# Optimization experiments

Measured on AMD Instinct MI355X. Metric: run time of the kernel, lower is better.

Reference implementation:

```python
import math
import jax, jax.numpy as jnp
import numpy as np

B, S, D = 4, 2048, 1024
L = 2                      # codec_decoder_transformer_lengths entry
H, HD = 8, 128             # n_heads == n_kv_heads (no GQA repeat)
FF = 4096
WINDOW = 16                # sliding window (causal: keys in [i-16, i])
NORM_EPS = 0.01
QK_EPS = 1e-6
SCALE_INIT = 0.1           # layer_id < 18 -> 0.1


def _alibi_slopes(n):
    # n is a power of 2 here (8)
    r = 2.0 ** (-8.0 / n)
    return jnp.array([r ** (i + 1) for i in range(n)], dtype=jnp.float32)


def rms_norm(x, w, eps):
    return x * jax.lax.rsqrt(jnp.mean(x * x, axis=-1, keepdims=True) + eps) * w


def _attn_bias(dtype):
    pos = jnp.arange(S)
    rel = pos[None, :] - pos[:, None]          # [S,S], rel = j - i
    slopes = _alibi_slopes(H).astype(dtype)
    bias = slopes[:, None, None] * rel[None].astype(dtype)   # [H,S,S]
    mask = (rel > 0) | (rel < -WINDOW)         # causal + sliding window
    return jnp.where(mask[None], -jnp.inf, bias)


def setup_inputs() -> dict:
    key = jax.random.key(0)
    ks = jax.random.split(key, 9)
    sd = 0.02
    w = lambda k, shape: jax.random.normal(k, shape, jnp.float32) * sd
    return {
        "x": jax.random.normal(ks[0], (B, S, D), jnp.float32),
        "wq": w(ks[1], (L, D, H * HD)),
        "wk": w(ks[2], (L, D, H * HD)),
        "wv": w(ks[3], (L, D, H * HD)),
        "wo": w(ks[4], (L, H * HD, D)),
        "q_norm_w": jnp.ones((L, H * HD), jnp.float32),
        "k_norm_w": jnp.ones((L, H * HD), jnp.float32),
        "w1": w(ks[5], (L, D, FF)),
        "w2": w(ks[6], (L, FF, D)),
        "w3": w(ks[7], (L, D, FF)),
        "attn_norm_w": jnp.ones((L, D), jnp.float32),
        "ffn_norm_w": jnp.ones((L, D), jnp.float32),
        "attn_scale": jnp.full((L, D), SCALE_INIT, jnp.float32),
        "ffn_scale": jnp.full((L, D), SCALE_INIT, jnp.float32),
    }


def reference(x, wq, wk, wv, wo, q_norm_w, k_norm_w, w1, w2, w3,
              attn_norm_w, ffn_norm_w, attn_scale, ffn_scale):
    bias = _attn_bias(x.dtype)                 # [H,S,S]
    inv_sqrt_d = 1.0 / math.sqrt(HD)

    def block(h, p):
        (lwq, lwk, lwv, lwo, qnw, knw, lw1, lw2, lw3, anw, fnw, asc, fsc) = p
        xn = rms_norm(h, anw, NORM_EPS)
        # qk_norm applied on the flat (H*HD) projection before the head split
        q = rms_norm(xn @ lwq, qnw, QK_EPS).reshape(B, S, H, HD).transpose(0, 2, 1, 3)
        k = rms_norm(xn @ lwk, knw, QK_EPS).reshape(B, S, H, HD).transpose(0, 2, 1, 3)
        v = (xn @ lwv).reshape(B, S, H, HD).transpose(0, 2, 1, 3)
        scores = jnp.einsum('bhqd,bhkd->bhqk', q, k) * inv_sqrt_d + bias[None]
        attn = jax.nn.softmax(scores, axis=-1)
        y = jnp.einsum('bhqk,bhkd->bhqd', attn, v)
        y = y.transpose(0, 2, 1, 3).reshape(B, S, H * HD)
        h = h + asc * (y @ lwo)
        xn = rms_norm(h, fnw, NORM_EPS)
        ff = (jax.nn.silu(xn @ lw1) * (xn @ lw3)) @ lw2
        return h + fsc * ff, None

    out, _ = jax.lax.scan(
        block, x,
        (wq, wk, wv, wo, q_norm_w, k_norm_w, w1, w2, w3,
         attn_norm_w, ffn_norm_w, attn_scale, ffn_scale))
    return out
```

## Files before the change

kernel.cpp:

```cpp
#include <hip/hip_runtime.h>

#define B_ 4
#define S_ 2048
#define D_ 1024
#define H_ 8
#define HD_ 128
#define FF_ 4096
#define R_ (B_*S_)

typedef __attribute__((ext_vector_type(8))) short short8;
typedef __attribute__((ext_vector_type(4))) float f32x4;

__device__ __forceinline__ unsigned short f2bf(float f) {
  unsigned int u = __float_as_uint(f);
  return (unsigned short)((u + 0x7fffu + ((u >> 16) & 1u)) >> 16);
}
__device__ __forceinline__ float bf2f(unsigned short s) {
  return __uint_as_float(((unsigned int)s) << 16);
}

typedef const __attribute__((address_space(1))) unsigned int* gas_p;
typedef __attribute__((address_space(3))) unsigned int* las_p;
__device__ __forceinline__ void gload16(const void* g, void* l) {
  __builtin_amdgcn_global_load_lds((gas_p)g, (las_p)l, 16, 0, 0);
}

__global__ __launch_bounds__(256) void f2bf_t(const float* __restrict__ src,
    unsigned short* __restrict__ dst, int Rows, int Cols) {
  __shared__ float tile[32][33];
  const int tx = threadIdx.x & 31, ty = threadIdx.x >> 5;
  const int r0 = blockIdx.y * 32, c0 = blockIdx.x * 32;
  #pragma unroll
  for (int j = 0; j < 32; j += 8)
    tile[ty + j][tx] = src[(size_t)(r0 + ty + j) * Cols + c0 + tx];
  __syncthreads();
  #pragma unroll
  for (int j = 0; j < 32; j += 8)
    dst[(size_t)(c0 + ty + j) * Rows + r0 + tx] = f2bf(tile[tx][ty + j]);
}

__global__ __launch_bounds__(256) void rmsnorm_f2b(const float* __restrict__ in,
    const float* __restrict__ w, unsigned short* __restrict__ out, float eps) {
  const int row = blockIdx.x, t = threadIdx.x;
  const float4 xv = *(const float4*)&in[(size_t)row * D_ + t * 4];
  float p = xv.x*xv.x + xv.y*xv.y + xv.z*xv.z + xv.w*xv.w;
  #pragma unroll
  for (int off = 32; off >= 1; off >>= 1) p += __shfl_xor(p, off);
  __shared__ float red[4];
  if ((t & 63) == 0) red[t >> 6] = p;
  __syncthreads();
  float scl = rsqrtf((red[0] + red[1] + red[2] + red[3]) * (1.0f / D_) + eps);
  const float4 wv = *(const float4*)&w[t * 4];
  ((ushort4*)out)[(size_t)row * 256 + t] = make_ushort4(
      f2bf(xv.x*scl*wv.x), f2bf(xv.y*scl*wv.y), f2bf(xv.z*scl*wv.z), f2bf(xv.w*scl*wv.w));
}

__global__ __launch_bounds__(256) void qknorm_k(unsigned short* __restrict__ qkv,
    const float* __restrict__ qw, const float* __restrict__ kw) {
  const int row = blockIdx.x, t = threadIdx.x;
  unsigned short* qp = qkv + (size_t)row * 3072;
  unsigned short* kp = qp + 1024;
  const ushort4 qv = ((const ushort4*)qp)[t];
  const ushort4 kv = ((const ushort4*)kp)[t];
  float q0 = bf2f(qv.x), q1 = bf2f(qv.y), q2 = bf2f(qv.z), q3 = bf2f(qv.w);
  float k0 = bf2f(kv.x), k1 = bf2f(kv.y), k2 = bf2f(kv.z), k3 = bf2f(kv.w);
  float pq = q0*q0 + q1*q1 + q2*q2 + q3*q3;
  float pk = k0*k0 + k1*k1 + k2*k2 + k3*k3;
  #pragma unroll
  for (int off = 32; off >= 1; off >>= 1) { pq += __shfl_xor(pq, off); pk += __shfl_xor(pk, off); }
  __shared__ float redq[4], redk[4];
  if ((t & 63) == 0) { redq[t >> 6] = pq; redk[t >> 6] = pk; }
  __syncthreads();
  float sq = rsqrtf((redq[0]+redq[1]+redq[2]+redq[3]) * (1.0f / D_) + 1e-6f);
  float sk = rsqrtf((redk[0]+redk[1]+redk[2]+redk[3]) * (1.0f / D_) + 1e-6f);
  const float4 qwv = *(const float4*)&qw[t * 4];
  const float4 kwv = *(const float4*)&kw[t * 4];
  ((ushort4*)qp)[t] = make_ushort4(f2bf(q0*sq*qwv.x), f2bf(q1*sq*qwv.y),
                                   f2bf(q2*sq*qwv.z), f2bf(q3*sq*qwv.w));
  ((ushort4*)kp)[t] = make_ushort4(f2bf(k0*sk*kwv.x), f2bf(k1*sk*kwv.y),
                                   f2bf(k2*sk*kwv.z), f2bf(k3*sk*kwv.w));
}

__global__ __launch_bounds__(256) void attn_k(const unsigned short* __restrict__ qkv,
    unsigned short* __restrict__ y) {
  const int lane = threadIdx.x & 63;
  const int wid = (blockIdx.x * 256 + threadIdx.x) >> 6;
  const int i  = wid & (S_ - 1);
  const int bh = wid >> 11;
  const int hh = bh & (H_ - 1);
  const int b  = bh >> 3;
  const float slope = exp2f(-(float)(hh + 1));
  const float inv = 0.088388347648318447f;
  const size_t rowq = ((size_t)(b * S_ + i)) * 3072 + hh * HD_ + lane * 2;
  const ushort2 qv = *(const ushort2*)&qkv[rowq];
  const float qx = bf2f(qv.x), qy = bf2f(qv.y);
  float sc[17];
  #pragma unroll
  for (int jj = 0; jj < 17; ++jj) {
    int j = i - 16 + jj;
    int jc = j < 0 ? 0 : j;
    size_t koff = ((size_t)(b * S_ + jc)) * 3072 + 1024 + hh * HD_ + lane * 2;
    ushort2 kv = *(const ushort2*)&qkv[koff];
    float p = qx * bf2f(kv.x) + qy * bf2f(kv.y);
    p += __shfl_xor(p, 32); p += __shfl_xor(p, 16); p += __shfl_xor(p, 8);
    p += __shfl_xor(p, 4);  p += __shfl_xor(p, 2);  p += __shfl_xor(p, 1);
    sc[jj] = (j >= 0) ? (p * inv + slope * (float)(jj - 16)) : -1e30f;
  }
  float m = sc[0];
  #pragma unroll
  for (int jj = 1; jj < 17; ++jj) m = fmaxf(m, sc[jj]);
  float wsum = 0.f, ax = 0.f, ay = 0.f;
  #pragma unroll
  for (int jj = 0; jj < 17; ++jj) {
    int j = i - 16 + jj;
    int jc = j < 0 ? 0 : j;
    float wgt = expf(sc[jj] - m);
    size_t voff = ((size_t)(b * S_ + jc)) * 3072 + 2048 + hh * HD_ + lane * 2;
    ushort2 vv = *(const ushort2*)&qkv[voff];
    wsum += wgt; ax += wgt * bf2f(vv.x); ay += wgt * bf2f(vv.y);
  }
  float rs = 1.f / wsum;
  size_t yoff = ((size_t)(b * S_ + i)) * 1024 + hh * HD_ + lane * 2;
  *(ushort2*)&y[yoff] = make_ushort2(f2bf(ax * rs), f2bf(ay * rs));
}

template<int EPI>
__global__ __launch_bounds__(512, 2) void gemm256(
    const unsigned short* __restrict__ A, const unsigned short* __restrict__ Bt,
    void* __restrict__ Cout, const float* __restrict__ sc, int M, int N, int K) {
  __shared__ __align__(16) unsigned short lds[2][2][16384];
  const int t = threadIdx.x;
  const int lane = t & 63, w = t >> 6;
  const int wm = w >> 2, wn = w & 3;
  const int lr = lane & 15, lk = lane >> 4;
  const int xm = lr & 7;

  const int nbx = N >> 8;
  const int nwg = gridDim.x;
  const int bid = blockIdx.x;
  const int swz = (bid & 7) * (nwg >> 3) + (bid >> 3);
  const int br = (swz / nbx) << 8;
  const int bc = (swz % nbx) << 8;

  const unsigned short* Abase = A + (size_t)br * K;
  const unsigned short* Bbase = Bt + (size_t)bc * K;

  auto stageA = [&](int buf, int u, int k0) {
    #pragma unroll
    for (int j = 0; j < 2; ++j) {
      int gr = (t + (j << 9)) >> 3, slot = t & 7;
      int row = ((gr & 63) | ((gr >> 6) << 7)) + (u << 6);
      gload16(Abase + (size_t)row * K + k0 + ((slot ^ (row & 7)) << 3),
              &lds[buf][0][row * 64 + slot * 8]);
    }
  };
  auto stageB = [&](int buf, int u, int k0) {
    #pragma unroll
    for (int j = 0; j < 2; ++j) {
      int gr = (t + (j << 9)) >> 3, slot = t & 7;
      int row = ((gr & 31) | ((gr >> 5) << 6)) + (u << 5);
      gload16(Bbase + (size_t)row * K + k0 + ((slot ^ (row & 7)) << 3),
              &lds[buf][1][row * 64 + slot * 8]);
    }
  };

  f32x4 acc[8][4];
  #pragma unroll
  for (int mi = 0; mi < 8; ++mi)
    #pragma unroll
    for (int ni = 0; ni < 4; ++ni) { f32x4 z = {0.f,0.f,0.f,0.f}; acc[mi][ni] = z; }

  const int NT = K >> 6;
  stageA(0, 0, 0); stageB(0, 0, 0); stageA(0, 1, 0); stageB(0, 1, 0);
  asm volatile("s_waitcnt vmcnt(0)" ::: "memory");
  __builtin_amdgcn_s_barrier();

  for (int kt = 0; kt < NT; ++kt) {
    const int cur = kt & 1, nxt = cur ^ 1;
    const int kp = (kt + 1 < NT) ? ((kt + 1) << 6) : 0;
    const unsigned short* Al = lds[cur][0];
    const unsigned short* Bl = lds[cur][1];
    short8 af[4][2], bfA[2][2], bfB[2][2];

    #pragma unroll
    for (int mf = 0; mf < 4; ++mf)
      #pragma unroll
      for (int ks = 0; ks < 2; ++ks)
        af[mf][ks] = *(const short8*)&Al[(wm*128 + mf*16 + lr)*64 + (((ks*4+lk)^xm)<<3)];
    #pragma unroll
    for (int nf = 0; nf < 2; ++nf)
      #pragma unroll
      for (int ks = 0; ks < 2; ++ks)
        bfA[nf][ks] = *(const short8*)&Bl[(wn*64 + nf*16 + lr)*64 + (((ks*4+lk)^xm)<<3)];
    stageA(nxt, 0, kp);
    asm volatile("s_waitcnt vmcnt(2)" ::: "memory");
    __builtin_amdgcn_s_barrier();
    asm volatile("s_waitcnt lgkmcnt(0)" ::: "memory");
    __builtin_amdgcn_sched_barrier(0);
    __builtin_amdgcn_s_setprio(1);
    #pragma unroll
    for (int mf = 0; mf < 4; ++mf)
      #pragma unroll
      for (int nf = 0; nf < 2; ++nf)
        #pragma unroll
        for (int ks = 0; ks < 2; ++ks)
          acc[mf][nf] = __builtin_amdgcn_mfma_f32_16x16x32_bf16(af[mf][ks], bfA[nf][ks], acc[mf][nf], 0, 0, 0);
    __builtin_amdgcn_s_setprio(0);
    __builtin_amdgcn_s_barrier();

    #pragma unroll
    for (int nf = 0; nf < 2; ++nf)
      #pragma unroll
      for (int ks = 0; ks < 2; ++ks)
        bfB[nf][ks] = *(const short8*)&Bl[(wn*64 + (nf+2)*16 + lr)*64 + (((ks*4+lk)^xm)<<3)];
    stageB(nxt, 0, kp);
    __builtin_amdgcn_s_barrier();
    asm volatile("s_waitcnt lgkmcnt(0)" ::: "memory");
    __builtin_amdgcn_sched_barrier(0);
    __builtin_amdgcn_s_setprio(1);
    #pragma unroll
    for (int mf = 0; mf < 4; ++mf)
      #pragma unroll
      for (int nf = 0; nf < 2; ++nf)
        #pragma unroll
        for (int ks = 0; ks < 2; ++ks)
          acc[mf][nf+2] = __builtin_amdgcn_mfma_f32_16x16x32_bf16(af[mf][ks], bfB[nf][ks], acc[mf][nf+2], 0, 0, 0);
    __builtin_amdgcn_s_setprio(0);
    __builtin_amdgcn_s_barrier();

    #pragma unroll
    for (int mf = 0; mf < 4; ++mf)
      #pragma unroll
      for (int ks = 0; ks < 2; ++ks)
        af[mf][ks] = *(const short8*)&Al[(wm*128 + (mf+4)*16 + lr)*64 + (((ks*4+lk)^xm)<<3)];
    stageA(nxt, 1, kp);
    __builtin_amdgcn_s_barrier();
    asm volatile("s_waitcnt lgkmcnt(0)" ::: "memory");
    __builtin_amdgcn_sched_barrier(0);
    __builtin_amdgcn_s_setprio(1);
    #pragma unroll
    for (int mf = 0; mf < 4; ++mf)
      #pragma unroll
      for (int nf = 0; nf < 2; ++nf)
        #pragma unroll
        for (int ks = 0; ks < 2; ++ks)
          acc[mf+4][nf+2] = __builtin_amdgcn_mfma_f32_16x16x32_bf16(af[mf][ks], bfB[nf][ks], acc[mf+4][nf+2], 0, 0, 0);
    __builtin_amdgcn_s_setprio(0);
    __builtin_amdgcn_s_barrier();

    #pragma unroll
    for (int nf = 0; nf < 2; ++nf)
      #pragma unroll
      for (int ks = 0; ks < 2; ++ks)
        bfA[nf][ks] = *(const short8*)&Bl[(wn*64 + nf*16 + lr)*64 + (((ks*4+lk)^xm)<<3)];
    stageB(nxt, 1, kp);
    asm volatile("s_waitcnt vmcnt(4)" ::: "memory");
    __builtin_amdgcn_s_barrier();
    asm volatile("s_waitcnt lgkmcnt(0)" ::: "memory");
    __builtin_amdgcn_sched_barrier(0);
    __builtin_amdgcn_s_setprio(1);
    #pragma unroll
    for (int mf = 0; mf < 4; ++mf)
      #pragma unroll
      for (int nf = 0; nf < 2; ++nf)
        #pragma unroll
        for (int ks = 0; ks < 2; ++ks)
          acc[mf+4][nf] = __builtin_amdgcn_mfma_f32_16x16x32_bf16(af[mf][ks], bfA[nf][ks], acc[mf+4][nf], 0, 0, 0);
    __builtin_amdgcn_s_setprio(0);
    __builtin_amdgcn_s_barrier();
  }

  if (EPI == 0) {
    unsigned short* C = (unsigned short*)Cout;
    #pragma unroll
    for (int mf = 0; mf < 8; ++mf)
      #pragma unroll
      for (int nf = 0; nf < 4; ++nf) {
        int row = br + wm*128 + mf*16 + lk*4;
        int col = bc + wn*64 + nf*16 + lr;
        #pragma unroll
        for (int r = 0; r < 4; ++r)
          C[(size_t)(row + r) * N + col] = f2bf(acc[mf][nf][r]);
      }
  } else {
    float* hp = (float*)Cout;
    #pragma unroll
    for (int nf = 0; nf < 4; ++nf) {
      int col = bc + wn*64 + nf*16 + lr;
      float sv = sc[col];
      #pragma unroll
      for (int mf = 0; mf < 8; ++mf) {
        int row = br + wm*128 + mf*16 + lk*4;
        #pragma unroll
        for (int r = 0; r < 4; ++r)
          hp[(size_t)(row + r) * N + col] += sv * acc[mf][nf][r];
      }
    }
  }
}

__device__ __forceinline__ void stage_tile(const unsigned short* __restrict__ src,
    unsigned short* lds, int rowbase, int K, int k0, int t) {
  #pragma unroll
  for (int it = 0; it < 4; ++it) {
    int g = it * 256 + t;
    int row = g >> 3, slot = g & 7;
    int sc8 = (slot ^ (row & 7)) << 3;
    gload16(&src[(size_t)(rowbase + row) * K + k0 + sc8], &lds[g * 8]);
  }
}

__global__ __launch_bounds__(256, 2) void gemm_w13(
    const unsigned short* __restrict__ A, const unsigned short* __restrict__ B1t,
    const unsigned short* __restrict__ B3t, unsigned short* __restrict__ G,
    int M, int N, int K) {
  __shared__ __align__(16) unsigned short As[128 * 64];
  __shared__ __align__(16) unsigned short B1s[128 * 64];
  __shared__ __align__(16) unsigned short B3s[128 * 64];
  const int t = threadIdx.x;
  const int lane = t & 63, w = t >> 6;
  const int wr = w >> 1, wc = w & 1;
  const int br = blockIdx.y * 128, bc = blockIdx.x * 128;
  const int lr = lane & 15, lk = lane >> 4;
  const int xm = lr & 7;
  f32x4 acc1[4][4], acc3[4][4];
  #pragma unroll
  for (int mi = 0; mi < 4; ++mi)
    #pragma unroll
    for (int ni = 0; ni < 4; ++ni) {
      f32x4 z = {0.f,0.f,0.f,0.f}; acc1[mi][ni] = z; acc3[mi][ni] = z;
    }
  for (int k0 = 0; k0 < K; k0 += 64) {
    stage_tile(A,   As,  br, K, k0, t);
    stage_tile(B1t, B1s, bc, K, k0, t);
    stage_tile(B3t, B3s, bc, K, k0, t);
    __syncthreads();
    #pragma unroll
    for (int kk = 0; kk < 2; ++kk) {
      short8 af[4], b1r[4], b3r[4];
      #pragma unroll
      for (int mi = 0; mi < 4; ++mi)
        af[mi] = *(const short8*)&As[(wr*64 + mi*16 + lr) * 64 + (((kk*4 + lk) ^ xm) << 3)];
      #pragma unroll
      for (int ni = 0; ni < 4; ++ni) {
        b1r[ni] = *(const short8*)&B1s[(wc*64 + ni*16 + lr) * 64 + (((kk*4 + lk) ^ xm) << 3)];
        b3r[ni] = *(const short8*)&B3s[(wc*64 + ni*16 + lr) * 64 + (((kk*4 + lk) ^ xm) << 3)];
      }
      #pragma unroll
      for (int mi = 0; mi < 4; ++mi)
        #pragma unroll
        for (int ni = 0; ni < 4; ++ni) {
          acc1[mi][ni] = __builtin_amdgcn_mfma_f32_16x16x32_bf16(af[mi], b1r[ni], acc1[mi][ni], 0, 0, 0);
          acc3[mi][ni] = __builtin_amdgcn_mfma_f32_16x16x32_bf16(af[mi], b3r[ni], acc3[mi][ni], 0, 0, 0);
        }
    }
    __syncthreads();
  }
  #pragma unroll
  for (int mi = 0; mi < 4; ++mi)
    #pragma unroll
    for (int ni = 0; ni < 4; ++ni) {
      int row = br + wr * 64 + mi * 16 + lk * 4;
      int col = bc + wc * 64 + ni * 16 + lr;
      #pragma unroll
      for (int r = 0; r < 4; ++r) {
        float a1 = acc1[mi][ni][r], a3 = acc3[mi][ni][r];
        G[(size_t)(row + r) * N + col] = f2bf(a1 / (1.f + expf(-a1)) * a3);
      }
    }
}

extern "C" void kernel_launch(void* const* d_in, const int* in_sizes, int n_in,
                              void* d_out, int out_size, void* d_ws, size_t ws_size,
                              hipStream_t stream) {
  const float* x    = (const float*)d_in[0];
  const float* wq   = (const float*)d_in[1];
  const float* wk   = (const float*)d_in[2];
  const float* wv   = (const float*)d_in[3];
  const float* wo   = (const float*)d_in[4];
  const float* qnw  = (const float*)d_in[5];
  const float* knw  = (const float*)d_in[6];
  const float* w1   = (const float*)d_in[7];
  const float* w2   = (const float*)d_in[8];
  const float* w3   = (const float*)d_in[9];
  const float* anw  = (const float*)d_in[10];
  const float* fnw  = (const float*)d_in[11];
  const float* asc  = (const float*)d_in[12];
  const float* fsc  = (const float*)d_in[13];

  const size_t MB = 1024 * 1024;
  if (ws_size < 144 * MB) return;

  float* h = (float*)d_out;
  char* ws = (char*)d_ws;
  unsigned short* qkvt = (unsigned short*)ws;
  unsigned short* wot  = qkvt + 2u * 3145728u;
  unsigned short* w1t  = wot  + 2u * 1048576u;
  unsigned short* w3t  = w1t  + 2u * 4194304u;
  unsigned short* w2t  = w3t  + 2u * 4194304u;
  unsigned short* xn   = (unsigned short*)(ws + 64 * MB);
  unsigned short* qkv  = (unsigned short*)(ws + 80 * MB);
  unsigned short* gate = qkv;

  hipMemcpyAsync(h, x, (size_t)R_ * D_ * sizeof(float), hipMemcpyDeviceToDevice, stream);

  for (int l = 0; l < 2; ++l) {
    unsigned short* qkvt_l = qkvt + (size_t)l * 3145728u;
    f2bf_t<<<dim3(32, 32),  256, 0, stream>>>(wq + (size_t)l*1048576, qkvt_l,            1024, 1024);
    f2bf_t<<<dim3(32, 32),  256, 0, stream>>>(wk + (size_t)l*1048576, qkvt_l + 1048576,  1024, 1024);
    f2bf_t<<<dim3(32, 32),  256, 0, stream>>>(wv + (size_t)l*1048576, qkvt_l + 2097152,  1024, 1024);
    f2bf_t<<<dim3(32, 32),  256, 0, stream>>>(wo + (size_t)l*1048576, wot + (size_t)l*1048576, 1024, 1024);
    f2bf_t<<<dim3(128, 32), 256, 0, stream>>>(w1 + (size_t)l*4194304, w1t + (size_t)l*4194304, 1024, 4096);
    f2bf_t<<<dim3(128, 32), 256, 0, stream>>>(w3 + (size_t)l*4194304, w3t + (size_t)l*4194304, 1024, 4096);
    f2bf_t<<<dim3(32, 128), 256, 0, stream>>>(w2 + (size_t)l*4194304, w2t + (size_t)l*4194304, 4096, 1024);
  }

  for (int l = 0; l < 2; ++l) {
    rmsnorm_f2b<<<R_, 256, 0, stream>>>(h, anw + l * D_, xn, 0.01f);
    gemm256<0><<<384, 512, 0, stream>>>(xn, qkvt + (size_t)l*3145728u, qkv, nullptr,
                                        R_, 3072, 1024);
    qknorm_k<<<R_, 256, 0, stream>>>(qkv, qnw + l * 1024, knw + l * 1024);
    attn_k<<<R_ * H_ / 4, 256, 0, stream>>>(qkv, xn);
    gemm256<1><<<128, 512, 0, stream>>>(xn, wot + (size_t)l*1048576u, h, asc + l * D_,
                                        R_, 1024, 1024);
    rmsnorm_f2b<<<R_, 256, 0, stream>>>(h, fnw + l * D_, xn, 0.01f);
    gemm_w13<<<dim3(32, 64), 256, 0, stream>>>(xn, w1t + (size_t)l*4194304u,
                                               w3t + (size_t)l*4194304u, gate, R_, 4096, 1024);
    gemm256<1><<<128, 512, 0, stream>>>(gate, w2t + (size_t)l*4194304u, h, fsc + l * D_,
                                        R_, 1024, 4096);
  }
}
```

Baseline: 1.016 ms.

## Merge weight conversions, shrink GEMM tiles to 256x128, rewrite W13 GEMM, drop memcpy

Replaces the fourteen per-matrix weight transpose/convert launches with a single kernel that covers both layers. The main GEMM tile changes from 256x256 to 256x128, which doubles the number of workgroups for the narrow N=1024 projections and gives a simpler double-buffered pipeline. The gated FFN GEMM gets a new 256x128 double-buffered version using direct global-to-LDS loads in place of the single-buffered 128x128 kernel. The initial x->h device copy is removed: layer 0 reads x directly and a new epilogue writes h = x + scale*acc. The smaller tiles trade more A-operand reloading for better occupancy and load balance.

```diff
diff --git a/kernel.cpp b/kernel.cpp
--- a/kernel.cpp
+++ b/kernel.cpp
@@ -25,11 +25,37 @@
   __builtin_amdgcn_global_load_lds((gas_p)g, (las_p)l, 16, 0, 0);
 }
 
-__global__ __launch_bounds__(256) void f2bf_t(const float* __restrict__ src,
-    unsigned short* __restrict__ dst, int Rows, int Cols) {
+__global__ __launch_bounds__(256) void f2bf_t_all(
+    const float* __restrict__ wq, const float* __restrict__ wk,
+    const float* __restrict__ wv, const float* __restrict__ wo,
+    const float* __restrict__ w1, const float* __restrict__ w3,
+    const float* __restrict__ w2,
+    unsigned short* __restrict__ qkvt, unsigned short* __restrict__ wot,
+    unsigned short* __restrict__ w1t, unsigned short* __restrict__ w3t,
+    unsigned short* __restrict__ w2t) {
+  const int id = blockIdx.x;
+  const int l = id >> 14, r = id & 16383;
+  const float* src; unsigned short* dst; int Rows, Cols, t2;
+  if (r < 4096) {
+    Rows = 1024; Cols = 1024; t2 = r & 1023;
+    const int wsel = r >> 10;
+    if (wsel == 0)      { src = wq + (size_t)l*1048576u; dst = qkvt + (size_t)l*3145728u; }
+    else if (wsel == 1) { src = wk + (size_t)l*1048576u; dst = qkvt + (size_t)l*3145728u + 1048576u; }
+    else if (wsel == 2) { src = wv + (size_t)l*1048576u; dst = qkvt + (size_t)l*3145728u + 2097152u; }
+    else                { src = wo + (size_t)l*1048576u; dst = wot + (size_t)l*1048576u; }
+  } else if (r < 12288) {
+    Rows = 1024; Cols = 4096; t2 = (r - 4096) & 4095;
+    if (r < 8192) { src = w1 + (size_t)l*4194304u; dst = w1t + (size_t)l*4194304u; }
+    else          { src = w3 + (size_t)l*4194304u; dst = w3t + (size_t)l*4194304u; }
+  } else {
+    Rows = 4096; Cols = 1024; t2 = r - 12288;
+    src = w2 + (size_t)l*4194304u; dst = w2t + (size_t)l*4194304u;
+  }
+  const int lgc = (Cols == 4096) ? 7 : 5;
+  const int bx = t2 & ((1 << lgc) - 1), by = t2 >> lgc;
+  const int r0 = by * 32, c0 = bx * 32;
   __shared__ float tile[32][33];
   const int tx = threadIdx.x & 31, ty = threadIdx.x >> 5;
-  const int r0 = blockIdx.y * 32, c0 = blockIdx.x * 32;
   #pragma unroll
   for (int j = 0; j < 32; j += 8)
     tile[ty + j][tx] = src[(size_t)(r0 + ty + j) * Cols + c0 + tx];
@@ -127,20 +153,22 @@
 template<int EPI>
 __global__ __launch_bounds__(512, 2) void gemm256(
     const unsigned short* __restrict__ A, const unsigned short* __restrict__ Bt,
-    void* __restrict__ Cout, const float* __restrict__ sc, int M, int N, int K) {
-  __shared__ __align__(16) unsigned short lds[2][2][16384];
+    void* __restrict__ Cout, const float* __restrict__ sc,
+    const float* __restrict__ x2, int M, int N, int K) {
+  __shared__ __align__(16) unsigned short ldsA[2][256 * 64];
+  __shared__ __align__(16) unsigned short ldsB[2][128 * 64];
   const int t = threadIdx.x;
   const int lane = t & 63, w = t >> 6;
   const int wm = w >> 2, wn = w & 3;
   const int lr = lane & 15, lk = lane >> 4;
   const int xm = lr & 7;
 
-  const int nbx = N >> 8;
+  const int nbx = N >> 7;
   const int nwg = gridDim.x;
   const int bid = blockIdx.x;
   const int swz = (bid & 7) * (nwg >> 3) + (bid >> 3);
   const int br = (swz / nbx) << 8;
-  const int bc = (swz % nbx) << 8;
+  const int bc = (swz % nbx) << 7;
 
   const unsigned short* Abase = A + (size_t)br * K;
   const unsigned short* Bbase = Bt + (size_t)bc * K;
@@ -148,52 +176,52 @@
   auto stageA = [&](int buf, int u, int k0) {
     #pragma unroll
     for (int j = 0; j < 2; ++j) {
-      int gr = (t + (j << 9)) >> 3, slot = t & 7;
+      int idx = t + (j << 9);
+      int gr = idx >> 3, slot = idx & 7;
       int row = ((gr & 63) | ((gr >> 6) << 7)) + (u << 6);
       gload16(Abase + (size_t)row * K + k0 + ((slot ^ (row & 7)) << 3),
-              &lds[buf][0][row * 64 + slot * 8]);
+              &ldsA[buf][row * 64 + slot * 8]);
     }
   };
-  auto stageB = [&](int buf, int u, int k0) {
+  auto stageB = [&](int buf, int k0) {
     #pragma unroll
     for (int j = 0; j < 2; ++j) {
-      int gr = (t + (j << 9)) >> 3, slot = t & 7;
-      int row = ((gr & 31) | ((gr >> 5) << 6)) + (u << 5);
+      int idx = t + (j << 9);
+      int row = idx >> 3, slot = idx & 7;
       gload16(Bbase + (size_t)row * K + k0 + ((slot ^ (row & 7)) << 3),
-              &lds[buf][1][row * 64 + slot * 8]);
+              &ldsB[buf][row * 64 + slot * 8]);
     }
   };
 
-  f32x4 acc[8][4];
+  f32x4 acc[8][2];
   #pragma unroll
   for (int mi = 0; mi < 8; ++mi)
     #pragma unroll
-    for (int ni = 0; ni < 4; ++ni) { f32x4 z = {0.f,0.f,0.f,0.f}; acc[mi][ni] = z; }
+    for (int ni = 0; ni < 2; ++ni) { f32x4 z = {0.f,0.f,0.f,0.f}; acc[mi][ni] = z; }
 
   const int NT = K >> 6;
-  stageA(0, 0, 0); stageB(0, 0, 0); stageA(0, 1, 0); stageB(0, 1, 0);
+  stageA(0, 0, 0); stageB(0, 0); stageA(0, 1, 0);
   asm volatile("s_waitcnt vmcnt(0)" ::: "memory");
   __builtin_amdgcn_s_barrier();
 
   for (int kt = 0; kt < NT; ++kt) {
     const int cur = kt & 1, nxt = cur ^ 1;
     const int kp = (kt + 1 < NT) ? ((kt + 1) << 6) : 0;
-    const unsigned short* Al = lds[cur][0];
-    const unsigned short* Bl = lds[cur][1];
-    short8 af[4][2], bfA[2][2], bfB[2][2];
-
-    #pragma unroll
-    for (int mf = 0; mf < 4; ++mf)
-      #pragma unroll
-      for (int ks = 0; ks < 2; ++ks)
-        af[mf][ks] = *(const short8*)&Al[(wm*128 + mf*16 + lr)*64 + (((ks*4+lk)^xm)<<3)];
-    #pragma unroll
-    for (int nf = 0; nf < 2; ++nf)
-      #pragma unroll
-      for (int ks = 0; ks < 2; ++ks)
-        bfA[nf][ks] = *(const short8*)&Bl[(wn*64 + nf*16 + lr)*64 + (((ks*4+lk)^xm)<<3)];
-    stageA(nxt, 0, kp);
-    asm volatile("s_waitcnt vmcnt(2)" ::: "memory");
+    const unsigned short* Al = ldsA[cur];
+    const unsigned short* Bl = ldsB[cur];
+    short8 af[2][4], bfr[2][2];
+
+    #pragma unroll
+    for (int ks = 0; ks < 2; ++ks) {
+      #pragma unroll
+      for (int mf = 0; mf < 4; ++mf)
+        af[ks][mf] = *(const short8*)&Al[(wm*128 + mf*16 + lr)*64 + (((ks*4+lk)^xm)<<3)];
+      #pragma unroll
+      for (int nf = 0; nf < 2; ++nf)
+        bfr[ks][nf] = *(const short8*)&Bl[(wn*32 + nf*16 + lr)*64 + (((ks*4+lk)^xm)<<3)];
+    }
+    stageA(nxt, 0, kp); stageB(nxt, kp); stageA(nxt, 1, kp);
+    asm volatile("s_waitcnt vmcnt(6)" ::: "memory");
     __builtin_amdgcn_s_barrier();
     asm volatile("s_waitcnt lgkmcnt(0)" ::: "memory");
     __builtin_amdgcn_sched_barrier(0);
@@ -204,16 +232,16 @@
       for (int nf = 0; nf < 2; ++nf)
         #pragma unroll
         for (int ks = 0; ks < 2; ++ks)
-          acc[mf][nf] = __builtin_amdgcn_mfma_f32_16x16x32_bf16(af[mf][ks], bfA[nf][ks], acc[mf][nf], 0, 0, 0);
+          acc[mf][nf] = __builtin_amdgcn_mfma_f32_16x16x32_bf16(af[ks][mf], bfr[ks][nf], acc[mf][nf], 0, 0, 0);
     __builtin_amdgcn_s_setprio(0);
     __builtin_amdgcn_s_barrier();
 
     #pragma unroll
-    for (int nf = 0; nf < 2; ++nf)
-      #pragma unroll
-      for (int ks = 0; ks < 2; ++ks)
-        bfB[nf][ks] = *(const short8*)&Bl[(wn*64 + (nf+2)*16 + lr)*64 + (((ks*4+lk)^xm)<<3)];
-    stageB(nxt, 0, kp);
+    for (int ks = 0; ks < 2; ++ks)
+      #pragma unroll
+      for (int mf = 0; mf < 4; ++mf)
+        af[ks][mf] = *(const short8*)&Al[(wm*128 + (mf+4)*16 + lr)*64 + (((ks*4+lk)^xm)<<3)];
+    asm volatile("s_waitcnt vmcnt(2)" ::: "memory");
     __builtin_amdgcn_s_barrier();
     asm volatile("s_waitcnt lgkmcnt(0)" ::: "memory");
     __builtin_amdgcn_sched_barrier(0);
@@ -224,16 +252,133 @@
       for (int nf = 0; nf < 2; ++nf)
         #pragma unroll
         for (int ks = 0; ks < 2; ++ks)
-          acc[mf][nf+2] = __builtin_amdgcn_mfma_f32_16x16x32_bf16(af[mf][ks], bfB[nf][ks], acc[mf][nf+2], 0, 0, 0);
+          acc[mf+4][nf] = __builtin_amdgcn_mfma_f32_16x16x32_bf16(af[ks][mf], bfr[ks][nf], acc[mf+4][nf], 0, 0, 0);
     __builtin_amdgcn_s_setprio(0);
     __builtin_amdgcn_s_barrier();
-
-    #pragma unroll
-    for (int mf = 0; mf < 4; ++mf)
-      #pragma unroll
-      for (int ks = 0; ks < 2; ++ks)
-        af[mf][ks] = *(const short8*)&Al[(wm*128 + (mf+4)*16 + lr)*64 + (((ks*4+lk)^xm)<<3)];
+  }
+
+  if (EPI == 0) {
+    unsigned short* C = (unsigned short*)Cout;
+    #pragma unroll
+    for (int mf = 0; mf < 8; ++mf)
+      #pragma unroll
+      for (int nf = 0; nf < 2; ++nf) {
+        int row = br + wm*128 + mf*16 + lk*4;
+        int col = bc + wn*32 + nf*16 + lr;
+        #pragma unroll
+        for (int r = 0; r < 4; ++r)
+          C[(size_t)(row + r) * N + col] = f2bf(acc[mf][nf][r]);
+      }
+  } else if (EPI == 1) {
+    float* hp = (float*)Cout;
+    #pragma unroll
+    for (int nf = 0; nf < 2; ++nf) {
+      int col = bc + wn*32 + nf*16 + lr;
+      float sv = sc[col];
+      #pragma unroll
+      for (int mf = 0; mf < 8; ++mf) {
+        int row = br + wm*128 + mf*16 + lk*4;
+        #pragma unroll
+        for (int r = 0; r < 4; ++r)
+          hp[(size_t)(row + r) * N + col] += sv * acc[mf][nf][r];
+      }
+    }
+  } else {
+    float* hp = (float*)Cout;
+    #pragma unroll
+    for (int nf = 0; nf < 2; ++nf) {
+      int col = bc + wn*32 + nf*16 + lr;
+      float sv = sc[col];
+      #pragma unroll
+      for (int mf = 0; mf < 8; ++mf) {
+        int row = br + wm*128 + mf*16 + lk*4;
+        #pragma unroll
+        for (int r = 0; r < 4; ++r)
+          hp[(size_t)(row + r) * N + col] = x2[(size_t)(row + r) * N + col] + sv * acc[mf][nf][r];
+      }
+    }
+  }
+}
+
+__global__ __launch_bounds__(512, 2) void gemm_w13_256(
+    const unsigned short* __restrict__ A, const unsigned short* __restrict__ B1t,
+    const unsigned short* __restrict__ B3t, unsigned short* __restrict__ G,
+    int M, int N, int K) {
+  __shared__ __align__(16) unsigned short ldsA[2][256 * 64];
+  __shared__ __align__(16) unsigned short ldsB1[2][128 * 64];
+  __shared__ __align__(16) unsigned short ldsB3[2][128 * 64];
+  const int t = threadIdx.x;
+  const int lane = t & 63, w = t >> 6;
+  const int wm = w >> 2, wn = w & 3;
+  const int lr = lane & 15, lk = lane >> 4;
+  const int xm = lr & 7;
+
+  const int nbx = N >> 7;
+  const int nwg = gridDim.x;
+  const int bid = blockIdx.x;
+  const int swz = (bid & 7) * (nwg >> 3) + (bid >> 3);
+  const int br = (swz / nbx) << 8;
+  const int bc = (swz % nbx) << 7;
+
+  const unsigned short* Abase  = A + (size_t)br * K;
+  const unsigned short* B1base = B1t + (size_t)bc * K;
+  const unsigned short* B3base = B3t + (size_t)bc * K;
+
+  auto stageA = [&](int buf, int u, int k0) {
+    #pragma unroll
+    for (int j = 0; j < 2; ++j) {
+      int idx = t + (j << 9);
+      int gr = idx >> 3, slot = idx & 7;
+      int row = ((gr & 63) | ((gr >> 6) << 7)) + (u << 6);
+      gload16(Abase + (size_t)row * K + k0 + ((slot ^ (row & 7)) << 3),
+              &ldsA[buf][row * 64 + slot * 8]);
+    }
+  };
+  auto stageB = [&](const unsigned short* Bb, unsigned short* ldsb, int k0) {
+    #pragma unroll
+    for (int j = 0; j < 2; ++j) {
+      int idx = t + (j << 9);
+      int row = idx >> 3, slot = idx & 7;
+      gload16(Bb + (size_t)row * K + k0 + ((slot ^ (row & 7)) << 3),
+              &ldsb[row * 64 + slot * 8]);
+    }
+  };
+
+  f32x4 acc1[8][2], acc3[8][2];
+  #pragma unroll
+  for (int mi = 0; mi < 8; ++mi)
+    #pragma unroll
+    for (int ni = 0; ni < 2; ++ni) {
+      f32x4 z = {0.f,0.f,0.f,0.f}; acc1[mi][ni] = z; acc3[mi][ni] = z;
+    }
+
+  const int NT = K >> 6;
+  stageA(0, 0, 0); stageB(B1base, ldsB1[0], 0); stageB(B3base, ldsB3[0], 0); stageA(0, 1, 0);
+  asm volatile("s_waitcnt vmcnt(0)" ::: "memory");
+  __builtin_amdgcn_s_barrier();
+
+  for (int kt = 0; kt < NT; ++kt) {
+    const int cur = kt & 1, nxt = cur ^ 1;
+    const int kp = (kt + 1 < NT) ? ((kt + 1) << 6) : 0;
+    const unsigned short* Al  = ldsA[cur];
+    const unsigned short* B1l = ldsB1[cur];
+    const unsigned short* B3l = ldsB3[cur];
+    short8 af[2][4], b1[2][2], b3[2][2];
+
+    #pragma unroll
+    for (int ks = 0; ks < 2; ++ks) {
+      #pragma unroll
+      for (int mf = 0; mf < 4; ++mf)
+        af[ks][mf] = *(const short8*)&Al[(wm*128 + mf*16 + lr)*64 + (((ks*4+lk)^xm)<<3)];
+      #pragma unroll
+      for (int nf = 0; nf < 2; ++nf) {
+        b1[ks][nf] = *(const short8*)&B1l[(wn*32 + nf*16 + lr)*64 + (((ks*4+lk)^xm)<<3)];
+        b3[ks][nf] = *(const short8*)&B3l[(wn*32 + nf*16 + lr)*64 + (((ks*4+lk)^xm)<<3)];
+      }
+    }
+    stageA(nxt, 0, kp); stageB(B1base, ldsB1[nxt], kp); stageB(B3base, ldsB3[nxt], kp);
     stageA(nxt, 1, kp);
+    asm volatile("s_waitcnt vmcnt(8)" ::: "memory");
     __builtin_amdgcn_s_barrier();
     asm volatile("s_waitcnt lgkmcnt(0)" ::: "memory");
     __builtin_amdgcn_sched_barrier(0);
@@ -243,18 +388,19 @@
       #pragma unroll
       for (int nf = 0; nf < 2; ++nf)
         #pragma unroll
-        for (int ks = 0; ks < 2; ++ks)
-          acc[mf+4][nf+2] = __builtin_amdgcn_mfma_f32_16x16x32_bf16(af[mf][ks], bfB[nf][ks], acc[mf+4][nf+2], 0, 0, 0);
+        for (int ks = 0; ks < 2; ++ks) {
+          acc1[mf][nf] = __builtin_amdgcn_mfma_f32_16x16x32_bf16(af[ks][mf], b1[ks][nf], acc1[mf][nf], 0, 0, 0);
+          acc3[mf][nf] = __builtin_amdgcn_mfma_f32_16x16x32_bf16(af[ks][mf], b3[ks][nf], acc3[mf][nf], 0, 0, 0);
+        }
     __builtin_amdgcn_s_setprio(0);
     __builtin_amdgcn_s_barrier();
 
     #pragma unroll
-    for (int nf = 0; nf < 2; ++nf)
-      #pragma unroll
-      for (int ks = 0; ks < 2; ++ks)
-        bfA[nf][ks] = *(const short8*)&Bl[(wn*64 + nf*16 + lr)*64 + (((ks*4+lk)^xm)<<3)];
-    stageB(nxt, 1, kp);
-    asm volatile("s_waitcnt vmcnt(4)" ::: "memory");
+    for (int ks = 0; ks < 2; ++ks)
+      #pragma unroll
+      for (int mf = 0; mf < 4; ++mf)
+        af[ks][mf] = *(const short8*)&Al[(wm*128 + (mf+4)*16 + lr)*64 + (((ks*4+lk)^xm)<<3)];
+    asm volatile("s_waitcnt vmcnt(2)" ::: "memory");
     __builtin_amdgcn_s_barrier();
     asm volatile("s_waitcnt lgkmcnt(0)" ::: "memory");
     __builtin_amdgcn_sched_barrier(0);
@@ -264,107 +410,23 @@
       #pragma unroll
       for (int nf = 0; nf < 2; ++nf)
         #pragma unroll
-        for (int ks = 0; ks < 2; ++ks)
-          acc[mf+4][nf] = __builtin_amdgcn_mfma_f32_16x16x32_bf16(af[mf][ks], bfA[nf][ks], acc[mf+4][nf], 0, 0, 0);
+        for (int ks = 0; ks < 2; ++ks) {
+          acc1[mf+4][nf] = __builtin_amdgcn_mfma_f32_16x16x32_bf16(af[ks][mf], b1[ks][nf], acc1[mf+4][nf], 0, 0, 0);
+          acc3[mf+4][nf] = __builtin_amdgcn_mfma_f32_16x16x32_bf16(af[ks][mf], b3[ks][nf], acc3[mf+4][nf], 0, 0, 0);
+        }
     __builtin_amdgcn_s_setprio(0);
     __builtin_amdgcn_s_barrier();
   }
 
-  if (EPI == 0) {
-    unsigned short* C = (unsigned short*)Cout;
-    #pragma unroll
-    for (int mf = 0; mf < 8; ++mf)
-      #pragma unroll
-      for (int nf = 0; nf < 4; ++nf) {
-        int row = br + wm*128 + mf*16 + lk*4;
-        int col = bc + wn*64 + nf*16 + lr;
-        #pragma unroll
-        for (int r = 0; r < 4; ++r)
-          C[(size_t)(row + r) * N + col] = f2bf(acc[mf][nf][r]);
-      }
-  } else {
-    float* hp = (float*)Cout;
-    #pragma unroll
-    for (int nf = 0; nf < 4; ++nf) {
-      int col = bc + wn*64 + nf*16 + lr;
-      float sv = sc[col];
-      #pragma unroll
-      for (int mf = 0; mf < 8; ++mf) {
-        int row = br + wm*128 + mf*16 + lk*4;
-        #pragma unroll
-        for (int r = 0; r < 4; ++r)
-          hp[(size_t)(row + r) * N + col] += sv * acc[mf][nf][r];
-      }
-    }
-  }
-}
-
-__device__ __forceinline__ void stage_tile(const unsigned short* __restrict__ src,
-    unsigned short* lds, int rowbase, int K, int k0, int t) {
-  #pragma unroll
-  for (int it = 0; it < 4; ++it) {
-    int g = it * 256 + t;
-    int row = g >> 3, slot = g & 7;
-    int sc8 = (slot ^ (row & 7)) << 3;
-    gload16(&src[(size_t)(rowbase + row) * K + k0 + sc8], &lds[g * 8]);
-  }
-}
-
-__global__ __launch_bounds__(256, 2) void gemm_w13(
-    const unsigned short* __restrict__ A, const unsigned short* __restrict__ B1t,
-    const unsigned short* __restrict__ B3t, unsigned short* __restrict__ G,
-    int M, int N, int K) {
-  __shared__ __align__(16) unsigned short As[128 * 64];
-  __shared__ __align__(16) unsigned short B1s[128 * 64];
-  __shared__ __align__(16) unsigned short B3s[128 * 64];
-  const int t = threadIdx.x;
-  const int lane = t & 63, w = t >> 6;
-  const int wr = w >> 1, wc = w & 1;
-  const int br = blockIdx.y * 128, bc = blockIdx.x * 128;
-  const int lr = lane & 15, lk = lane >> 4;
-  const int xm = lr & 7;
-  f32x4 acc1[4][4], acc3[4][4];
-  #pragma unroll
-  for (int mi = 0; mi < 4; ++mi)
-    #pragma unroll
-    for (int ni = 0; ni < 4; ++ni) {
-      f32x4 z = {0.f,0.f,0.f,0.f}; acc1[mi][ni] = z; acc3[mi][ni] = z;
-    }
-  for (int k0 = 0; k0 < K; k0 += 64) {
-    stage_tile(A,   As,  br, K, k0, t);
-    stage_tile(B1t, B1s, bc, K, k0, t);
-    stage_tile(B3t, B3s, bc, K, k0, t);
-    __syncthreads();
-    #pragma unroll
-    for (int kk = 0; kk < 2; ++kk) {
-      short8 af[4], b1r[4], b3r[4];
-      #pragma unroll
-      for (int mi = 0; mi < 4; ++mi)
-        af[mi] = *(const short8*)&As[(wr*64 + mi*16 + lr) * 64 + (((kk*4 + lk) ^ xm) << 3)];
-      #pragma unroll
-      for (int ni = 0; ni < 4; ++ni) {
-        b1r[ni] = *(const short8*)&B1s[(wc*64 + ni*16 + lr) * 64 + (((kk*4 + lk) ^ xm) << 3)];
-        b3r[ni] = *(const short8*)&B3s[(wc*64 + ni*16 + lr) * 64 + (((kk*4 + lk) ^ xm) << 3)];
-      }
-      #pragma unroll
-      for (int mi = 0; mi < 4; ++mi)
-        #pragma unroll
-        for (int ni = 0; ni < 4; ++ni) {
-          acc1[mi][ni] = __builtin_amdgcn_mfma_f32_16x16x32_bf16(af[mi], b1r[ni], acc1[mi][ni], 0, 0, 0);
-          acc3[mi][ni] = __builtin_amdgcn_mfma_f32_16x16x32_bf16(af[mi], b3r[ni], acc3[mi][ni], 0, 0, 0);
-        }
-    }
-    __syncthreads();
-  }
-  #pragma unroll
-  for (int mi = 0; mi < 4; ++mi)
-    #pragma unroll
-    for (int ni = 0; ni < 4; ++ni) {
-      int row = br + wr * 64 + mi * 16 + lk * 4;
-      int col = bc + wc * 64 + ni * 16 + lr;
+  #pragma unroll
+  for (int mf = 0; mf < 8; ++mf)
+    #pragma unroll
+    for (int nf = 0; nf < 2; ++nf) {
+      int row = br + wm*128 + mf*16 + lk*4;
+      int col = bc + wn*32 + nf*16 + lr;
       #pragma unroll
       for (int r = 0; r < 4; ++r) {
-        float a1 = acc1[mi][ni][r], a3 = acc3[mi][ni][r];
+        float a1 = acc1[mf][nf][r], a3 = acc3[mf][nf][r];
         G[(size_t)(row + r) * N + col] = f2bf(a1 / (1.f + expf(-a1)) * a3);
       }
     }
@@ -402,31 +464,24 @@
   unsigned short* qkv  = (unsigned short*)(ws + 80 * MB);
   unsigned short* gate = qkv;
 
-  hipMemcpyAsync(h, x, (size_t)R_ * D_ * sizeof(float), hipMemcpyDeviceToDevice, stream);
+  f2bf_t_all<<<32768, 256, 0, stream>>>(wq, wk, wv, wo, w1, w3, w2,
+                                        qkvt, wot, w1t, w3t, w2t);
 
   for (int l = 0; l < 2; ++l) {
-    unsigned short* qkvt_l = qkvt + (size_t)l * 3145728u;
-    f2bf_t<<<dim3(32, 32),  256, 0, stream>>>(wq + (size_t)l*1048576, qkvt_l,            1024, 1024);
-    f2bf_t<<<dim3(32, 32),  256, 0, stream>>>(wk + (size_t)l*1048576, qkvt_l + 1048576,  1024, 1024);
-    f2bf_t<<<dim3(32, 32),  256, 0, stream>>>(wv + (size_t)l*1048576, qkvt_l + 2097152,  1024, 1024);
-    f2bf_t<<<dim3(32, 32),  256, 0, stream>>>(wo + (size_t)l*1048576, wot + (size_t)l*1048576, 1024, 1024);
-    f2bf_t<<<dim3(128, 32), 256, 0, stream>>>(w1 + (size_t)l*4194304, w1t + (size_t)l*4194304, 1024, 4096);
-    f2bf_t<<<dim3(128, 32), 256, 0, stream>>>(w3 + (size_t)l*4194304, w3t + (size_t)l*4194304, 1024, 4096);
-    f2bf_t<<<dim3(32, 128), 256, 0, stream>>>(w2 + (size_t)l*4194304, w2t + (size_t)l*4194304, 4096, 1024);
-  }
-
-  for (int l = 0; l < 2; ++l) {
-    rmsnorm_f2b<<<R_, 256, 0, stream>>>(h, anw + l * D_, xn, 0.01f);
-    gemm256<0><<<384, 512, 0, stream>>>(xn, qkvt + (size_t)l*3145728u, qkv, nullptr,
+    rmsnorm_f2b<<<R_, 256, 0, stream>>>(l == 0 ? x : h, anw + l * D_, xn, 0.01f);
+    gemm256<0><<<768, 512, 0, stream>>>(xn, qkvt + (size_t)l*3145728u, qkv, nullptr, nullptr,
                                         R_, 3072, 1024);
     qknorm_k<<<R_, 256, 0, stream>>>(qkv, qnw + l * 1024, knw + l * 1024);
     attn_k<<<R_ * H_ / 4, 256, 0, stream>>>(qkv, xn);
-    gemm256<1><<<128, 512, 0, stream>>>(xn, wot + (size_t)l*1048576u, h, asc + l * D_,
-                                        R_, 1024, 1024);
+    if (l == 0)
+      gemm256<2><<<256, 512, 0, stream>>>(xn, wot, h, asc, x, R_, 1024, 1024);
+    else
+      gemm256<1><<<256, 512, 0, stream>>>(xn, wot + 1048576u, h, asc + D_, nullptr,
+                                          R_, 1024, 1024);
     rmsnorm_f2b<<<R_, 256, 0, stream>>>(h, fnw + l * D_, xn, 0.01f);
-    gemm_w13<<<dim3(32, 64), 256, 0, stream>>>(xn, w1t + (size_t)l*4194304u,
-                                               w3t + (size_t)l*4194304u, gate, R_, 4096, 1024);
-    gemm256<1><<<128, 512, 0, stream>>>(gate, w2t + (size_t)l*4194304u, h, fsc + l * D_,
-                                        R_, 1024, 4096);
-  }
-}
+    gemm_w13_256<<<1024, 512, 0, stream>>>(xn, w1t + (size_t)l*4194304u,
+                                           w3t + (size_t)l*4194304u, gate, R_, 4096, 1024);
+    gemm256<1><<<256, 512, 0, stream>>>(gate, w2t + (size_t)l*4194304u, h, fsc + l * D_,
+                                        nullptr, R_, 1024, 4096);
+  }
+}
```

After: 970.1 us. 1.05x faster.
